# Performance work log

Measured on AMD Instinct MI355X. Metric: run time of the kernel, lower is better.

The kernel has to match this reference:

```python
import jax, jax.numpy as jnp
import numpy as np

N = 4096
D = 256
TAU = 0.8
LAM = 0.5
K0, K1 = 64, 128


def setup_inputs() -> dict:
    key = jax.random.key(0)
    ks = jax.random.split(key, 20)
    s = 1.0 / np.sqrt(D)
    pos = (jax.random.uniform(ks[3], (N, N)) < 0.01).astype(jnp.float32)
    pos = pos.at[jnp.arange(N), jnp.arange(N)].set(1.0)  # guarantee a positive per row
    return {
        'z_mp': jax.random.normal(ks[0], (N, D), jnp.float32),
        'z_sc': jax.random.normal(ks[1], (N, D), jnp.float32),
        'feat': jax.random.normal(ks[2], (N, D), jnp.float32),
        'pos': pos,
        'im2c0': jax.random.randint(ks[4], (N,), 0, K0, jnp.int32),
        'im2c1': jax.random.randint(ks[5], (N,), 0, K1, jnp.int32),
        'centroids0': jax.random.normal(ks[6], (K0, D), jnp.float32),
        'centroids1': jax.random.normal(ks[7], (K1, D), jnp.float32),
        'density0': jax.random.uniform(ks[8], (K0,), jnp.float32) + 0.5,
        'density1': jax.random.uniform(ks[9], (K1,), jnp.float32) + 0.5,
        'pW1': jax.random.normal(ks[10], (D, D), jnp.float32) * s * 1.414,
        'pb1': jnp.zeros((D,), jnp.float32),
        'pW2': jax.random.normal(ks[11], (D, D), jnp.float32) * s * 1.414,
        'pb2': jnp.zeros((D,), jnp.float32),
        'mW1': jax.random.normal(ks[12], (D, D), jnp.float32) * s,
        'mb1': jnp.zeros((D,), jnp.float32),
        'mW2': jax.random.normal(ks[13], (D, D), jnp.float32) * s,
        'mb2': jnp.zeros((D,), jnp.float32),
    }


def _mlp(x, W1, b1, W2, b2):
    # nn.Linear -> ELU -> nn.Linear (torch Linear: x @ W.T + b)
    return jax.nn.elu(x @ W1.T + b1) @ W2.T + b2


def _sim(z1, z2, tau):
    n1 = jnp.linalg.norm(z1, axis=-1, keepdims=True)
    n2 = jnp.linalg.norm(z2, axis=-1, keepdims=True)
    return jnp.exp((z1 @ z2.T) / (n1 @ n2.T) / tau)


def _nce(sim_matrix, pos):
    m = sim_matrix / (sim_matrix.sum(axis=1, keepdims=True) + 1e-8)
    return -jnp.log((m * pos).sum(axis=-1)).mean()


def _pocl(z_anchor, z, im2cs, centroids, densities):
    n = z_anchor.shape[0]
    # weight[a,b] = #levels where a,b share a cluster (original: coo @ coo.T summed)
    sames = [(c[:, None] == c[None, :]).astype(z.dtype) for c in im2cs]
    weight = sames[0] + sames[1]
    node_prototypes = jnp.zeros_like(z)
    loss = jnp.float32(0.0)
    for same, im2c, protos, dens in zip(sames, im2cs, centroids, densities):
        # original aliases weight_clus = weight, so masking accumulates in-place
        weight = weight * same
        c = (weight @ z) / weight.sum(axis=1)[:, None]
        node_prototypes = node_prototypes + 0.1 * c
        phi = dens[im2c]
        pos_p = jnp.exp((z_anchor * node_prototypes).sum(axis=1) / phi)
        neg_p = jnp.exp((z_anchor @ protos.T) / dens).mean(axis=1) * n
        loss = loss + (-jnp.log(pos_p / neg_p)).mean()
    return loss / len(im2cs)


def reference(z_mp, z_sc, feat, pos, im2c0, im2c1, centroids0, centroids1,
              density0, density1, pW1, pb1, pW2, pb2, mW1, mb1, mW2, mb2):
    z_proj_mp = _mlp(z_mp, pW1, pb1, pW2, pb2)
    z_proj_sc = _mlp(z_sc, pW1, pb1, pW2, pb2)
    m_mp2sc = _sim(z_proj_mp, z_proj_sc, TAU)
    lori_mp = _nce(m_mp2sc, pos)
    lori_sc = _nce(m_mp2sc.T, pos)
    proto_loss = _pocl(z_sc, z_mp, [im2c0, im2c1],
                       [centroids0, centroids1], [density0, density1])
    mp_intra = _mlp(z_mp, mW1, mb1, mW2, mb2)
    loss_intramp = _nce(_sim(mp_intra, mp_intra, 0.05), pos)
    proj_mp_feat = _mlp(z_mp, pW1, pb1, pW2, pb2)
    proj_feat = _mlp(feat, pW1, pb1, pW2, pb2)
    lori_mpfeat = _nce(_sim(proj_mp_feat, proj_feat, TAU), pos)
    lori_featmp = _nce(_sim(proj_feat, proj_mp_feat, TAU), pos)
    return (LAM * lori_mp + (1 - LAM) * lori_sc + 0.3 * loss_intramp
            + proto_loss + 0.01 * lori_mpfeat + 0.01 * lori_featmp)
```

## Files before the change

### kernel.cpp

```cpp
#include <hip/hip_runtime.h>
#include <math.h>


#define NROWS 4096
#define DIM   256
#define ND    ((size_t)NROWS * DIM)

typedef unsigned short u16;
typedef unsigned int   u32;
typedef unsigned long long u64;
typedef __attribute__((ext_vector_type(8))) short bf16x8;
typedef __attribute__((ext_vector_type(4))) float f32x4;

__device__ __forceinline__ u16 f2bf(float f) {
    u32 u = __float_as_uint(f);
    return (u16)((u + 0x7fffu + ((u >> 16) & 1u)) >> 16);
}
__device__ __forceinline__ float bf2f(u16 h) {
    return __uint_as_float(((u32)h) << 16);
}

__device__ __forceinline__ void gload16(const u16* g, u16* l) {
    __builtin_amdgcn_global_load_lds(
        (const __attribute__((address_space(1))) u32*)g,
        (__attribute__((address_space(3))) u32*)l, 16, 0, 0);
}

template<int ROWS>
__device__ __forceinline__ void stage_panel(const u16* P, int kk, u16* S, int tid) {
#pragma unroll
    for (int p = 0; p < ROWS / 64; ++p) {
        const int ch = p * 256 + tid, row = ch >> 2, seg = ch & 3;
        gload16(P + (size_t)row * DIM + kk + seg * 8, &S[ch * 8]);
    }
}

__device__ __forceinline__ void wait_lgkm0() {
    asm volatile("s_waitcnt lgkmcnt(0)" ::: "memory");
    __builtin_amdgcn_sched_barrier(0);
}
template<int N> __device__ __forceinline__ void wait_vm() {
    if constexpr (N == 0)      asm volatile("s_waitcnt vmcnt(0)" ::: "memory");
    else if constexpr (N == 3) asm volatile("s_waitcnt vmcnt(3)" ::: "memory");
    else if constexpr (N == 4) asm volatile("s_waitcnt vmcnt(4)" ::: "memory");
}

struct PreArgs {
    const float* in0; const float* in1; const float* in2;
    const float* w0; const float* w1; const float* w2; const float* w3;
    const float* c0; const float* c1;
    const float* pos; const float* z_mp;
    const int* im0; const int* im1;
};
__global__ __launch_bounds__(256) void fused_pre(PreArgs p,
                                                 u16* __restrict__ INb,
                                                 u16* __restrict__ Wb,
                                                 u16* __restrict__ CB,
                                                 u64* __restrict__ bits,
                                                 float* __restrict__ S01,
                                                 float* __restrict__ cnt01)
{
    const int b = blockIdx.x, tid = threadIdx.x;
    if (b < 3072) {
        const int z = b >> 10;
        const float* s = z == 0 ? p.in0 : (z == 1 ? p.in1 : p.in2);
        const int i = (b & 1023) * 256 + tid;
        const float4 v = ((const float4*)s)[i];
        ushort4 o;
        o.x = f2bf(v.x); o.y = f2bf(v.y); o.z = f2bf(v.z); o.w = f2bf(v.w);
        ((ushort4*)(INb + (size_t)z * ND))[i] = o;
    } else if (b < 3328) {
        const int q = b - 3072, wi = q >> 6;
        const float* s = wi == 0 ? p.w0 : (wi == 1 ? p.w1 : (wi == 2 ? p.w2 : p.w3));
        const int i = (q & 63) * 256 + tid;
        const float4 v = ((const float4*)s)[i];
        ushort4 o;
        o.x = f2bf(v.x); o.y = f2bf(v.y); o.z = f2bf(v.z); o.w = f2bf(v.w);
        ((ushort4*)(Wb + (size_t)wi * 65536))[i] = o;
    } else if (b < 3376) {
        const int i = (b - 3328) * 256 + tid;
        const float4 v = (i < 4096) ? ((const float4*)p.c0)[i]
                                    : ((const float4*)p.c1)[i - 4096];
        ushort4 o;
        o.x = f2bf(v.x); o.y = f2bf(v.y); o.z = f2bf(v.z); o.w = f2bf(v.w);
        ((ushort4*)CB)[i] = o;
    } else if (b < 7472) {
        const int i = b - 3376;
        const int w = tid >> 6, l = tid & 63;
#pragma unroll
        for (int c = 0; c < 16; ++c) {
            const int j = c * 256 + w * 64 + l;
            const float v = p.pos[(size_t)i * NROWS + j];
            const u64 m = __ballot(v != 0.f);
            if (l == 0) bits[(size_t)i * 64 + c * 4 + w] = m;
        }
    } else {
        const int r = b - 7472;
        const int pp = p.im0[r] * 128 + p.im1[r];
        atomicAdd(&S01[(size_t)pp * DIM + tid], p.z_mp[(size_t)r * DIM + tid]);
        if (tid == 0) atomicAdd(&cnt01[pp], 1.f);
    }
}

template<int ACT, int REMAP, int SQ>
__global__ __launch_bounds__(256, 4) void mlp_mfma(const u16* __restrict__ IN,
                                                   const u16* __restrict__ Wp,
                                                   const u16* __restrict__ Wm,
                                                   const float* __restrict__ bp,
                                                   const float* __restrict__ bm,
                                                   u16* __restrict__ OUT,
                                                   float* __restrict__ SS)
{
    __shared__ __align__(16) u16 As[3][64 * 32];
    __shared__ __align__(16) u16 Bs[3][128 * 32];
    const int tid = threadIdx.x;
    const int bx = blockIdx.x, by = blockIdx.y;
    const bool intra = by >= 192;
    const int arow = (REMAP && intra) ? (by - 192) * 64 : by * 64;
    const u16* A = IN + (size_t)arow * DIM;
    const u16* B = (intra ? Wm : Wp) + (size_t)(bx * 128) * DIM;
    const float* bias = intra ? bm : bp;
    const int l = tid & 63, w = tid >> 6, wr = w >> 1, wc = w & 1;
    const int lr = l & 15, lk = l >> 4;

    f32x4 acc[2][4] = {};
    stage_panel<64>(A, 0, As[0], tid);
    stage_panel<128>(B, 0, Bs[0], tid);
    stage_panel<64>(A, 32, As[1], tid);
    stage_panel<128>(B, 32, Bs[1], tid);
    wait_vm<3>();
    __builtin_amdgcn_s_barrier();
#pragma unroll
    for (int t = 0; t < 8; ++t) {
        bf16x8 a[2], b[4];
#pragma unroll
        for (int mi = 0; mi < 2; ++mi)
            a[mi] = *(const bf16x8*)&As[t % 3][(wr * 32 + mi * 16 + lr) * 32 + lk * 8];
#pragma unroll
        for (int ni = 0; ni < 4; ++ni)
            b[ni] = *(const bf16x8*)&Bs[t % 3][(wc * 64 + ni * 16 + lr) * 32 + lk * 8];
        if (t < 6) {
            stage_panel<64>(A, (t + 2) * 32, As[(t + 2) % 3], tid);
            stage_panel<128>(B, (t + 2) * 32, Bs[(t + 2) % 3], tid);
        }
        wait_lgkm0();
#pragma unroll
        for (int mi = 0; mi < 2; ++mi)
#pragma unroll
            for (int ni = 0; ni < 4; ++ni)
                acc[mi][ni] = __builtin_amdgcn_mfma_f32_16x16x32_bf16(a[mi], b[ni], acc[mi][ni], 0, 0, 0);
        if (t < 6)      { wait_vm<3>(); __builtin_amdgcn_s_barrier(); }
        else if (t < 7) { wait_vm<0>(); __builtin_amdgcn_s_barrier(); }
    }

    const int j0 = bx * 128;
    float bv[4];
#pragma unroll
    for (int ni = 0; ni < 4; ++ni) bv[ni] = bias[j0 + wc * 64 + ni * 16 + lr];
#pragma unroll
    for (int mi = 0; mi < 2; ++mi)
#pragma unroll
        for (int r = 0; r < 4; ++r) {
            const int row = by * 64 + wr * 32 + mi * 16 + lk * 4 + r;
            float v4[4], sq = 0.f;
#pragma unroll
            for (int ni = 0; ni < 4; ++ni) {
                float v = acc[mi][ni][r] + bv[ni];
                if (ACT) v = v > 0.f ? v : expm1f(v);
                v4[ni] = v;
                sq += v * v;
            }
            if (SQ) {
#pragma unroll
                for (int m = 1; m < 16; m <<= 1) sq += __shfl_xor(sq, m);
                if (lr == 0) atomicAdd(&SS[row], sq);
            }
#pragma unroll
            for (int ni = 0; ni < 4; ++ni)
                OUT[(size_t)row * DIM + j0 + wc * 64 + ni * 16 + lr] = f2bf(v4[ni]);
        }
}

__global__ __launch_bounds__(256, 3) void simstat3c(const u16* __restrict__ PROJ,
                                                    const u64* __restrict__ bits,
                                                    const float* __restrict__ SS,
                                                    float* __restrict__ ST)
{
    const int bid = blockIdx.x;
    int z, by, bx;
    if (bid < 1024) {
        z = 0;
        const int x = bid & 7, j = bid >> 3;
        by = (x >> 1) * 8 + (j >> 4);
        bx = (x & 1) * 16 + (j & 15);
    } else if (bid < 1552) {
        z = 1;
        const int u = bid - 1024;
        const int t = (u & 7) * 66 + (u >> 3);
        int r = (int)((65.0f - sqrtf(4225.0f - 8.0f * (float)t)) * 0.5f);
        int off = 32 * r - (r * (r - 1)) / 2;
        if (t < off)                   { --r; off -= 33 - r; }
        else if (t >= off + (32 - r))  { off += 32 - r; ++r; }
        by = r; bx = r + (t - off);
    } else {
        z = 2;
        const int v = bid - 1552;
        const int x = v & 7, j = v >> 3;
        by = (x >> 1) * 8 + (j >> 4);
        bx = (x & 1) * 16 + (j & 15);
    }

    __shared__ __align__(16) u16 As[3][128 * 32];
    __shared__ __align__(16) u16 Bs[3][128 * 32];
    const int tid = threadIdx.x;
    int ao, bo;
    float* rsr; float* rsc;
    switch (z) {
        case 0:  ao = 0; bo = 1; rsr = ST + 0;     rsc = ST + 8192;  break;
        case 1:  ao = 3; bo = 3; rsr = ST + 16384; rsc = ST + 16384; break;
        default: ao = 0; bo = 2; rsr = ST + 24576; rsc = ST + 32768; break;
    }
    const float invtau = (z == 1) ? 20.f : 1.25f;
    const bool docol = (z != 1) || (bx > by);
    const int i0 = by * 128, j0 = bx * 128;
    const u16* A = PROJ + (size_t)ao * ND + (size_t)i0 * DIM;
    const u16* B = PROJ + (size_t)bo * ND + (size_t)j0 * DIM;
    const int l = tid & 63, w = tid >> 6, wr = w >> 1, wc = w & 1;
    const int lr = l & 15, lk = l >> 4;

    f32x4 acc[4][4] = {};
    stage_panel<128>(A, 0, As[0], tid);
    stage_panel<128>(B, 0, Bs[0], tid);
    stage_panel<128>(A, 32, As[1], tid);
    stage_panel<128>(B, 32, Bs[1], tid);
    wait_vm<4>();
    __builtin_amdgcn_s_barrier();
#pragma unroll
    for (int t = 0; t < 8; ++t) {
        bf16x8 a[4], b[4];
#pragma unroll
        for (int mi = 0; mi < 4; ++mi)
            a[mi] = *(const bf16x8*)&As[t % 3][(wr * 64 + mi * 16 + lr) * 32 + lk * 8];
#pragma unroll
        for (int ni = 0; ni < 4; ++ni)
            b[ni] = *(const bf16x8*)&Bs[t % 3][(wc * 64 + ni * 16 + lr) * 32 + lk * 8];
        if (t < 6) {
            stage_panel<128>(A, (t + 2) * 32, As[(t + 2) % 3], tid);
            stage_panel<128>(B, (t + 2) * 32, Bs[(t + 2) % 3], tid);
        }
        wait_lgkm0();
#pragma unroll
        for (int mi = 0; mi < 4; ++mi)
#pragma unroll
            for (int ni = 0; ni < 4; ++ni)
                acc[mi][ni] = __builtin_amdgcn_mfma_f32_16x16x32_bf16(a[mi], b[ni], acc[mi][ni], 0, 0, 0);
        if (t < 6)      { wait_vm<4>(); __builtin_amdgcn_s_barrier(); }
        else if (t < 7) { wait_vm<0>(); __builtin_amdgcn_s_barrier(); }
    }

    const float* ssa = SS + ao * 4096;
    const float* ssb = SS + bo * 4096;
    float ri[4][4], rj[4];
#pragma unroll
    for (int mi = 0; mi < 4; ++mi)
#pragma unroll
        for (int r = 0; r < 4; ++r)
            ri[mi][r] = rsqrtf(ssa[i0 + wr * 64 + mi * 16 + lk * 4 + r]) * invtau;
#pragma unroll
    for (int ni = 0; ni < 4; ++ni)
        rj[ni] = rsqrtf(ssb[j0 + wc * 64 + ni * 16 + lr]);
#pragma unroll
    for (int mi = 0; mi < 4; ++mi)
#pragma unroll
        for (int ni = 0; ni < 4; ++ni)
#pragma unroll
            for (int r = 0; r < 4; ++r)
                acc[mi][ni][r] = __expf(acc[mi][ni][r] * ri[mi][r] * rj[ni]);

#pragma unroll
    for (int mi = 0; mi < 4; ++mi)
#pragma unroll
        for (int r = 0; r < 4; ++r) {
            const int i = i0 + wr * 64 + mi * 16 + lk * 4 + r;
            const u64 pw = bits[(size_t)i * 64 + bx * 2 + wc];
            float rsum = 0.f, psum = 0.f;
#pragma unroll
            for (int ni = 0; ni < 4; ++ni) {
                const float ev = acc[mi][ni][r];
                rsum += ev;
                psum += ((pw >> (ni * 16 + lr)) & 1ull) ? ev : 0.f;
            }
#pragma unroll
            for (int m = 1; m < 16; m <<= 1) {
                rsum += __shfl_xor(rsum, m);
                psum += __shfl_xor(psum, m);
            }
            if (lr == 0) {
                atomicAdd(&rsr[i], rsum);
                atomicAdd(&rsr[4096 + i], psum);
            }
        }

    if (docol) {
#pragma unroll
        for (int ni = 0; ni < 4; ++ni) {
            const int j = j0 + wc * 64 + ni * 16 + lr;
            const u64 pw = bits[(size_t)j * 64 + by * 2 + wr];
            float csum = 0.f, qsum = 0.f;
#pragma unroll
            for (int mi = 0; mi < 4; ++mi)
#pragma unroll
                for (int r = 0; r < 4; ++r) {
                    const float ev = acc[mi][ni][r];
                    csum += ev;
                    qsum += ((pw >> (mi * 16 + lk * 4 + r)) & 1ull) ? ev : 0.f;
                }
            csum += __shfl_xor(csum, 16); csum += __shfl_xor(csum, 32);
            qsum += __shfl_xor(qsum, 16); qsum += __shfl_xor(qsum, 32);
            if (lk == 0) {
                atomicAdd(&rsc[j], csum);
                atomicAdd(&rsc[4096 + j], qsum);
            }
        }
    }
}

__global__ __launch_bounds__(256, 4) void gcent_mfma(const u16* __restrict__ Zb,
                                                     const u16* __restrict__ CB,
                                                     float* __restrict__ G)
{
    __shared__ __align__(16) u16 As[3][128 * 32];
    __shared__ __align__(16) u16 Bs[3][64 * 32];
    const int tid = threadIdx.x;
    const int bx = blockIdx.x, by = blockIdx.y;
    const int i0 = by * 128, j0 = bx * 64;
    const u16* A = Zb + (size_t)i0 * DIM;
    const u16* B = CB + (size_t)j0 * DIM;
    const int l = tid & 63, w = tid >> 6, wr = w >> 1, wc = w & 1;
    const int lr = l & 15, lk = l >> 4;

    f32x4 acc[4][2] = {};
    stage_panel<128>(A, 0, As[0], tid);
    stage_panel<64>(B, 0, Bs[0], tid);
    stage_panel<128>(A, 32, As[1], tid);
    stage_panel<64>(B, 32, Bs[1], tid);
    wait_vm<3>();
    __builtin_amdgcn_s_barrier();
#pragma unroll
    for (int t = 0; t < 8; ++t) {
        bf16x8 a[4], b[2];
#pragma unroll
        for (int mi = 0; mi < 4; ++mi)
            a[mi] = *(const bf16x8*)&As[t % 3][(wr * 64 + mi * 16 + lr) * 32 + lk * 8];
#pragma unroll
        for (int ni = 0; ni < 2; ++ni)
            b[ni] = *(const bf16x8*)&Bs[t % 3][(wc * 32 + ni * 16 + lr) * 32 + lk * 8];
        if (t < 6) {
            stage_panel<128>(A, (t + 2) * 32, As[(t + 2) % 3], tid);
            stage_panel<64>(B, (t + 2) * 32, Bs[(t + 2) % 3], tid);
        }
        wait_lgkm0();
#pragma unroll
        for (int mi = 0; mi < 4; ++mi)
#pragma unroll
            for (int ni = 0; ni < 2; ++ni)
                acc[mi][ni] = __builtin_amdgcn_mfma_f32_16x16x32_bf16(a[mi], b[ni], acc[mi][ni], 0, 0, 0);
        if (t < 6)      { wait_vm<3>(); __builtin_amdgcn_s_barrier(); }
        else if (t < 7) { wait_vm<0>(); __builtin_amdgcn_s_barrier(); }
    }

#pragma unroll
    for (int mi = 0; mi < 4; ++mi)
#pragma unroll
        for (int r = 0; r < 4; ++r) {
            const int row = i0 + wr * 64 + mi * 16 + lk * 4 + r;
#pragma unroll
            for (int ni = 0; ni < 2; ++ni)
                G[(size_t)row * 192 + j0 + wc * 32 + ni * 16 + lr] = acc[mi][ni][r];
        }
}

__global__ __launch_bounds__(256) void reduce_pairs(const float* __restrict__ S01,
                                                    const float* __restrict__ cnt01,
                                                    float* __restrict__ S0,
                                                    float* __restrict__ cnt0)
{
    const int k0 = blockIdx.x, d = threadIdx.x;
    float s = 0.f;
    for (int k1 = 0; k1 < 128; ++k1)
        s += S01[(size_t)(k0 * 128 + k1) * DIM + d];
    S0[(size_t)k0 * DIM + d] = s;
    __shared__ float c[128];
    if (d < 128) c[d] = cnt01[k0 * 128 + d];
    __syncthreads();
    if (d == 0) {
        float t = 0.f;
        for (int i = 0; i < 128; ++i) t += c[i];
        cnt0[k0] = t;
    }
}

__global__ __launch_bounds__(256) void pocl_row(const float* __restrict__ z_sc,
                                                const int* __restrict__ i0a,
                                                const int* __restrict__ i1a,
                                                const float* __restrict__ S0,
                                                const float* __restrict__ S01,
                                                const float* __restrict__ cnt0,
                                                const float* __restrict__ cnt01,
                                                const float* __restrict__ G,
                                                const float* __restrict__ d0,
                                                const float* __restrict__ d1,
                                                float* __restrict__ L1,
                                                float* __restrict__ L2)
{
    const int w = threadIdx.x >> 6, l = threadIdx.x & 63;
    const int a = blockIdx.x * 4 + w;
    const int k0 = i0a[a], k1 = i1a[a];
    const int p = k0 * 128 + k1;
    const float n0 = cnt0[k0], n01 = cnt01[p];
    const float inv1 = 1.f / (n0 + n01), inv2 = 1.f / n01;
    const float4 s0  = *(const float4*)&S0[(size_t)k0 * DIM + l * 4];
    const float4 s01 = *(const float4*)&S01[(size_t)p * DIM + l * 4];
    const float4 zd  = *(const float4*)&z_sc[(size_t)a * DIM + l * 4];

    float dot1 = 0.f, dot2 = 0.f;
    {
        const float c1x = (s0.x + s01.x) * inv1, c2x = s01.x * inv2;
        const float c1y = (s0.y + s01.y) * inv1, c2y = s01.y * inv2;
        const float c1z = (s0.z + s01.z) * inv1, c2z = s01.z * inv2;
        const float c1w = (s0.w + s01.w) * inv1, c2w = s01.w * inv2;
        dot1 = zd.x * c1x + zd.y * c1y + zd.z * c1z + zd.w * c1w;
        dot2 = zd.x * (c1x + c2x) + zd.y * (c1y + c2y) + zd.z * (c1z + c2z) + zd.w * (c1w + c2w);
    }
    dot1 *= 0.1f; dot2 *= 0.1f;
#pragma unroll
    for (int m = 1; m < 64; m <<= 1) {
        dot1 += __shfl_xor(dot1, m);
        dot2 += __shfl_xor(dot2, m);
    }

    const float x0 = G[(size_t)a * 192 + l] / d0[l];
    float M0 = x0;
#pragma unroll
    for (int m = 1; m < 64; m <<= 1) M0 = fmaxf(M0, __shfl_xor(M0, m));
    float e0 = __expf(x0 - M0);
#pragma unroll
    for (int m = 1; m < 64; m <<= 1) e0 += __shfl_xor(e0, m);

    const float x1a = G[(size_t)a * 192 + 64 + l] / d1[l];
    const float x1b = G[(size_t)a * 192 + 128 + l] / d1[64 + l];
    float M1 = fmaxf(x1a, x1b);
#pragma unroll
    for (int m = 1; m < 64; m <<= 1) M1 = fmaxf(M1, __shfl_xor(M1, m));
    float e1 = __expf(x1a - M1) + __expf(x1b - M1);
#pragma unroll
    for (int m = 1; m < 64; m <<= 1) e1 += __shfl_xor(e1, m);

    if (l == 0) {
        const float lneg1 = M0 + logf(e0) - logf(64.f)  + logf(4096.f);
        const float lneg2 = M1 + logf(e1) - logf(128.f) + logf(4096.f);
        L1[a] = lneg1 - dot1 / d0[k0];
        L2[a] = lneg2 - dot2 / d1[k1];
    }
}

__global__ __launch_bounds__(256) void final_reduce(const float* __restrict__ st,
                                                    const float* __restrict__ L1,
                                                    const float* __restrict__ L2,
                                                    float* __restrict__ out)
{
    const int t = threadIdx.x;
    const float* rs0 = st + 0;      const float* pr0 = st + 4096;
    const float* rs1 = st + 8192;   const float* pr1 = st + 12288;
    const float* rs2 = st + 16384;  const float* pr2 = st + 20480;
    const float* rs3 = st + 24576;  const float* pr3 = st + 28672;
    const float* rs4 = st + 32768;  const float* pr4 = st + 36864;

    float acc = 0.f;
    for (int i = t; i < NROWS; i += 256) {
        const float lmp = logf(rs0[i] + 1e-8f) - logf(pr0[i]);
        const float lsc = logf(rs1[i] + 1e-8f) - logf(pr1[i]);
        const float lin = logf(rs2[i] + 1e-8f) - logf(pr2[i]);
        const float lmf = logf(rs3[i] + 1e-8f) - logf(pr3[i]);
        const float lfm = logf(rs4[i] + 1e-8f) - logf(pr4[i]);
        acc += 0.5f * (lmp + lsc) + 0.3f * lin
             + 0.01f * (lmf + lfm) + 0.5f * (L1[i] + L2[i]);
    }
    __shared__ float red[256];
    red[t] = acc; __syncthreads();
    for (int s = 128; s > 0; s >>= 1) {
        if (t < s) red[t] += red[t + s];
        __syncthreads();
    }
    if (t == 0) out[0] = red[0] * (1.f / 4096.f);
}

extern "C" void kernel_launch(void* const* d_in, const int* in_sizes, int n_in,
                              void* d_out, int out_size, void* d_ws, size_t ws_size,
                              hipStream_t stream)
{
    const float* z_mp = (const float*)d_in[0];
    const float* z_sc = (const float*)d_in[1];
    const float* feat = (const float*)d_in[2];
    const float* pos  = (const float*)d_in[3];
    const int*   im0  = (const int*)d_in[4];
    const int*   im1  = (const int*)d_in[5];
    const float* c0   = (const float*)d_in[6];
    const float* c1   = (const float*)d_in[7];
    const float* d0   = (const float*)d_in[8];
    const float* d1   = (const float*)d_in[9];
    const float* pW1  = (const float*)d_in[10];
    const float* pb1  = (const float*)d_in[11];
    const float* pW2  = (const float*)d_in[12];
    const float* pb2  = (const float*)d_in[13];
    const float* mW1  = (const float*)d_in[14];
    const float* mb1  = (const float*)d_in[15];
    const float* mW2  = (const float*)d_in[16];
    const float* mb2  = (const float*)d_in[17];
    float* out = (float*)d_out;
    float* ws  = (float*)d_ws;
    (void)in_sizes; (void)n_in; (void)out_size; (void)ws_size;

    float* ST   = ws;
    float* S0f  = ST + 40960;
    float* CN0  = S0f + 16384;
    float* CN01 = CN0 + 64;
    float* S01f = CN01 + 8192;
    float* SS   = S01f + (size_t)8192 * DIM;
    float* ZEND = SS + 16384;
    float* G    = ZEND;
    float* L1   = G + (size_t)NROWS * 192;
    float* L2   = L1 + NROWS;
    u64*  bits  = (u64*)(L2 + NROWS);
    u16*  INb   = (u16*)(bits + (size_t)NROWS * 64);
    u16*  Hb    = INb + 3 * ND;
    u16*  PROJ  = Hb + 4 * ND;
    u16*  Wb    = PROJ + 4 * ND;
    u16*  CB    = Wb + 4 * 65536;

    hipMemsetAsync(ws, 0, (size_t)(ZEND - ws) * sizeof(float), stream);

    const dim3 blk(256);

    PreArgs pa{z_mp, z_sc, feat, pW1, pW2, mW1, mW2, c0, c1, pos, z_mp, im0, im1};
    fused_pre<<<11568, blk, 0, stream>>>(pa, INb, Wb, CB, bits, S01f, CN01);

    mlp_mfma<1, 1, 0><<<dim3(2, 256), blk, 0, stream>>>(INb, Wb, Wb + 2 * 65536,
                                                        pb1, mb1, Hb, nullptr);
    mlp_mfma<0, 0, 1><<<dim3(2, 256), blk, 0, stream>>>(Hb, Wb + 65536, Wb + 3 * 65536,
                                                        pb2, mb2, PROJ, SS);

    simstat3c<<<2576, blk, 0, stream>>>(PROJ, bits, SS, ST);

    reduce_pairs<<<64, blk, 0, stream>>>(S01f, CN01, S0f, CN0);
    gcent_mfma<<<dim3(3, 32), blk, 0, stream>>>(INb + ND, CB, G);
    pocl_row<<<1024, blk, 0, stream>>>(z_sc, im0, im1, S0f, S01f, CN0, CN01,
                                       G, d0, d1, L1, L2);

    final_reduce<<<1, blk, 0, stream>>>(ST, L1, L2, out);
}
```

Measured before the change: 156.7 us.

## Merge independent small kernels into two combined launches and use DPP row sums

```diff
diff --git a/kernel.cpp b/kernel.cpp
--- a/kernel.cpp
+++ b/kernel.cpp
@@ -43,6 +43,14 @@
     if constexpr (N == 0)      asm volatile("s_waitcnt vmcnt(0)" ::: "memory");
     else if constexpr (N == 3) asm volatile("s_waitcnt vmcnt(3)" ::: "memory");
     else if constexpr (N == 4) asm volatile("s_waitcnt vmcnt(4)" ::: "memory");
+}
+
+__device__ __forceinline__ float rowsum16(float v) {
+    v += __int_as_float(__builtin_amdgcn_update_dpp(0, __float_as_int(v), 0x118, 0xf, 0xf, true));
+    v += __int_as_float(__builtin_amdgcn_update_dpp(0, __float_as_int(v), 0x114, 0xf, 0xf, true));
+    v += __int_as_float(__builtin_amdgcn_update_dpp(0, __float_as_int(v), 0x112, 0xf, 0xf, true));
+    v += __int_as_float(__builtin_amdgcn_update_dpp(0, __float_as_int(v), 0x111, 0xf, 0xf, true));
+    return v;
 }
 
 struct PreArgs {
@@ -103,18 +111,17 @@
 }
 
 template<int ACT, int REMAP, int SQ>
-__global__ __launch_bounds__(256, 4) void mlp_mfma(const u16* __restrict__ IN,
-                                                   const u16* __restrict__ Wp,
-                                                   const u16* __restrict__ Wm,
-                                                   const float* __restrict__ bp,
-                                                   const float* __restrict__ bm,
-                                                   u16* __restrict__ OUT,
-                                                   float* __restrict__ SS)
-{
-    __shared__ __align__(16) u16 As[3][64 * 32];
-    __shared__ __align__(16) u16 Bs[3][128 * 32];
-    const int tid = threadIdx.x;
-    const int bx = blockIdx.x, by = blockIdx.y;
+__device__ __forceinline__ void mlp_body(int bx, int by, u16* lds, int tid,
+                                         const u16* __restrict__ IN,
+                                         const u16* __restrict__ Wp,
+                                         const u16* __restrict__ Wm,
+                                         const float* __restrict__ bp,
+                                         const float* __restrict__ bm,
+                                         u16* __restrict__ OUT,
+                                         float* __restrict__ SS)
+{
+    u16* As = lds;
+    u16* Bs = lds + 3 * 2048;
     const bool intra = by >= 192;
     const int arow = (REMAP && intra) ? (by - 192) * 64 : by * 64;
     const u16* A = IN + (size_t)arow * DIM;
@@ -124,10 +131,10 @@
     const int lr = l & 15, lk = l >> 4;
 
     f32x4 acc[2][4] = {};
-    stage_panel<64>(A, 0, As[0], tid);
-    stage_panel<128>(B, 0, Bs[0], tid);
-    stage_panel<64>(A, 32, As[1], tid);
-    stage_panel<128>(B, 32, Bs[1], tid);
+    stage_panel<64>(A, 0, As, tid);
+    stage_panel<128>(B, 0, Bs, tid);
+    stage_panel<64>(A, 32, As + 2048, tid);
+    stage_panel<128>(B, 32, Bs + 4096, tid);
     wait_vm<3>();
     __builtin_amdgcn_s_barrier();
 #pragma unroll
@@ -135,13 +142,13 @@
         bf16x8 a[2], b[4];
 #pragma unroll
         for (int mi = 0; mi < 2; ++mi)
-            a[mi] = *(const bf16x8*)&As[t % 3][(wr * 32 + mi * 16 + lr) * 32 + lk * 8];
+            a[mi] = *(const bf16x8*)&As[(t % 3) * 2048 + (wr * 32 + mi * 16 + lr) * 32 + lk * 8];
 #pragma unroll
         for (int ni = 0; ni < 4; ++ni)
-            b[ni] = *(const bf16x8*)&Bs[t % 3][(wc * 64 + ni * 16 + lr) * 32 + lk * 8];
+            b[ni] = *(const bf16x8*)&Bs[(t % 3) * 4096 + (wc * 64 + ni * 16 + lr) * 32 + lk * 8];
         if (t < 6) {
-            stage_panel<64>(A, (t + 2) * 32, As[(t + 2) % 3], tid);
-            stage_panel<128>(B, (t + 2) * 32, Bs[(t + 2) % 3], tid);
+            stage_panel<64>(A, (t + 2) * 32, As + ((t + 2) % 3) * 2048, tid);
+            stage_panel<128>(B, (t + 2) * 32, Bs + ((t + 2) % 3) * 4096, tid);
         }
         wait_lgkm0();
 #pragma unroll
@@ -171,14 +178,187 @@
                 sq += v * v;
             }
             if (SQ) {
-#pragma unroll
-                for (int m = 1; m < 16; m <<= 1) sq += __shfl_xor(sq, m);
-                if (lr == 0) atomicAdd(&SS[row], sq);
+                sq = rowsum16(sq);
+                if (lr == 15) atomicAdd(&SS[row], sq);
             }
 #pragma unroll
             for (int ni = 0; ni < 4; ++ni)
                 OUT[(size_t)row * DIM + j0 + wc * 64 + ni * 16 + lr] = f2bf(v4[ni]);
         }
+}
+
+__device__ __forceinline__ void gcent_body(int bx, int by, u16* lds, int tid,
+                                           const u16* __restrict__ Zb,
+                                           const u16* __restrict__ CB,
+                                           float* __restrict__ G)
+{
+    u16* As = lds;
+    u16* Bs = lds + 3 * 4096;
+    const int i0 = by * 128, j0 = bx * 64;
+    const u16* A = Zb + (size_t)i0 * DIM;
+    const u16* B = CB + (size_t)j0 * DIM;
+    const int l = tid & 63, w = tid >> 6, wr = w >> 1, wc = w & 1;
+    const int lr = l & 15, lk = l >> 4;
+
+    f32x4 acc[4][2] = {};
+    stage_panel<128>(A, 0, As, tid);
+    stage_panel<64>(B, 0, Bs, tid);
+    stage_panel<128>(A, 32, As + 4096, tid);
+    stage_panel<64>(B, 32, Bs + 2048, tid);
+    wait_vm<3>();
+    __builtin_amdgcn_s_barrier();
+#pragma unroll
+    for (int t = 0; t < 8; ++t) {
+        bf16x8 a[4], b[2];
+#pragma unroll
+        for (int mi = 0; mi < 4; ++mi)
+            a[mi] = *(const bf16x8*)&As[(t % 3) * 4096 + (wr * 64 + mi * 16 + lr) * 32 + lk * 8];
+#pragma unroll
+        for (int ni = 0; ni < 2; ++ni)
+            b[ni] = *(const bf16x8*)&Bs[(t % 3) * 2048 + (wc * 32 + ni * 16 + lr) * 32 + lk * 8];
+        if (t < 6) {
+            stage_panel<128>(A, (t + 2) * 32, As + ((t + 2) % 3) * 4096, tid);
+            stage_panel<64>(B, (t + 2) * 32, Bs + ((t + 2) % 3) * 2048, tid);
+        }
+        wait_lgkm0();
+#pragma unroll
+        for (int mi = 0; mi < 4; ++mi)
+#pragma unroll
+            for (int ni = 0; ni < 2; ++ni)
+                acc[mi][ni] = __builtin_amdgcn_mfma_f32_16x16x32_bf16(a[mi], b[ni], acc[mi][ni], 0, 0, 0);
+        if (t < 6)      { wait_vm<3>(); __builtin_amdgcn_s_barrier(); }
+        else if (t < 7) { wait_vm<0>(); __builtin_amdgcn_s_barrier(); }
+    }
+
+#pragma unroll
+    for (int mi = 0; mi < 4; ++mi)
+#pragma unroll
+        for (int r = 0; r < 4; ++r) {
+            const int row = i0 + wr * 64 + mi * 16 + lk * 4 + r;
+#pragma unroll
+            for (int ni = 0; ni < 2; ++ni)
+                G[(size_t)row * 192 + j0 + wc * 32 + ni * 16 + lr] = acc[mi][ni][r];
+        }
+}
+
+__device__ __forceinline__ void pocl_body(int blk, int tid,
+                                          const float* __restrict__ z_sc,
+                                          const int* __restrict__ i0a,
+                                          const int* __restrict__ i1a,
+                                          const float* __restrict__ S0,
+                                          const float* __restrict__ S01,
+                                          const float* __restrict__ cnt0,
+                                          const float* __restrict__ cnt01,
+                                          const float* __restrict__ G,
+                                          const float* __restrict__ d0,
+                                          const float* __restrict__ d1,
+                                          float* __restrict__ L1,
+                                          float* __restrict__ L2)
+{
+    const int w = tid >> 6, l = tid & 63;
+    const int a = blk * 4 + w;
+    const int k0 = i0a[a], k1 = i1a[a];
+    const int p = k0 * 128 + k1;
+    const float n0 = cnt0[k0], n01 = cnt01[p];
+    const float inv1 = 1.f / (n0 + n01), inv2 = 1.f / n01;
+    const float4 s0  = *(const float4*)&S0[(size_t)k0 * DIM + l * 4];
+    const float4 s01 = *(const float4*)&S01[(size_t)p * DIM + l * 4];
+    const float4 zd  = *(const float4*)&z_sc[(size_t)a * DIM + l * 4];
+
+    float dot1 = 0.f, dot2 = 0.f;
+    {
+        const float c1x = (s0.x + s01.x) * inv1, c2x = s01.x * inv2;
+        const float c1y = (s0.y + s01.y) * inv1, c2y = s01.y * inv2;
+        const float c1z = (s0.z + s01.z) * inv1, c2z = s01.z * inv2;
+        const float c1w = (s0.w + s01.w) * inv1, c2w = s01.w * inv2;
+        dot1 = zd.x * c1x + zd.y * c1y + zd.z * c1z + zd.w * c1w;
+        dot2 = zd.x * (c1x + c2x) + zd.y * (c1y + c2y) + zd.z * (c1z + c2z) + zd.w * (c1w + c2w);
+    }
+    dot1 *= 0.1f; dot2 *= 0.1f;
+#pragma unroll
+    for (int m = 1; m < 64; m <<= 1) {
+        dot1 += __shfl_xor(dot1, m);
+        dot2 += __shfl_xor(dot2, m);
+    }
+
+    const float x0 = G[(size_t)a * 192 + l] / d0[l];
+    float M0 = x0;
+#pragma unroll
+    for (int m = 1; m < 64; m <<= 1) M0 = fmaxf(M0, __shfl_xor(M0, m));
+    float e0 = __expf(x0 - M0);
+#pragma unroll
+    for (int m = 1; m < 64; m <<= 1) e0 += __shfl_xor(e0, m);
+
+    const float x1a = G[(size_t)a * 192 + 64 + l] / d1[l];
+    const float x1b = G[(size_t)a * 192 + 128 + l] / d1[64 + l];
+    float M1 = fmaxf(x1a, x1b);
+#pragma unroll
+    for (int m = 1; m < 64; m <<= 1) M1 = fmaxf(M1, __shfl_xor(M1, m));
+    float e1 = __expf(x1a - M1) + __expf(x1b - M1);
+#pragma unroll
+    for (int m = 1; m < 64; m <<= 1) e1 += __shfl_xor(e1, m);
+
+    if (l == 0) {
+        const float lneg1 = M0 + logf(e0) - logf(64.f)  + logf(4096.f);
+        const float lneg2 = M1 + logf(e1) - logf(128.f) + logf(4096.f);
+        L1[a] = lneg1 - dot1 / d0[k0];
+        L2[a] = lneg2 - dot2 / d1[k1];
+    }
+}
+
+struct C1Args {
+    const u16* INb; const u16* Wb; const u16* CB;
+    const float* pb1; const float* mb1;
+    u16* Hb; float* G;
+    const float* S01; const float* cnt01; float* S0; float* cnt0;
+};
+__global__ __launch_bounds__(256, 4) void combo1(C1Args a)
+{
+    extern __shared__ u16 smem[];
+    const int b = blockIdx.x, tid = threadIdx.x;
+    if (b < 512) {
+        mlp_body<1, 1, 0>(b & 1, b >> 1, smem, tid, a.INb, a.Wb, a.Wb + 2 * 65536,
+                          a.pb1, a.mb1, a.Hb, nullptr);
+    } else if (b < 608) {
+        const int q = b - 512;
+        gcent_body(q % 3, q / 3, smem, tid, a.INb + ND, a.CB, a.G);
+    } else {
+        const int k0 = b - 608, d = tid;
+        float s = 0.f;
+        for (int k1 = 0; k1 < 128; ++k1)
+            s += a.S01[(size_t)(k0 * 128 + k1) * DIM + d];
+        a.S0[(size_t)k0 * DIM + d] = s;
+        float* c = (float*)smem;
+        if (d < 128) c[d] = a.cnt01[k0 * 128 + d];
+        __syncthreads();
+        if (d == 0) {
+            float t = 0.f;
+            for (int i = 0; i < 128; ++i) t += c[i];
+            a.cnt0[k0] = t;
+        }
+    }
+}
+
+struct C2Args {
+    const u16* Hb; const u16* Wb;
+    const float* pb2; const float* mb2;
+    u16* PROJ; float* SS;
+    const float* z_sc; const int* im0; const int* im1;
+    const float* S0; const float* S01; const float* cnt0; const float* cnt01;
+    const float* G; const float* d0; const float* d1;
+    float* L1; float* L2;
+};
+__global__ __launch_bounds__(256, 4) void combo2(C2Args a)
+{
+    extern __shared__ u16 smem[];
+    const int b = blockIdx.x, tid = threadIdx.x;
+    if (b < 512) {
+        mlp_body<0, 0, 1>(b & 1, b >> 1, smem, tid, a.Hb, a.Wb + 65536,
+                          a.Wb + 3 * 65536, a.pb2, a.mb2, a.PROJ, a.SS);
+    } else {
+        pocl_body(b - 512, tid, a.z_sc, a.im0, a.im1, a.S0, a.S01, a.cnt0,
+                  a.cnt01, a.G, a.d0, a.d1, a.L1, a.L2);
+    }
 }
 
 __global__ __launch_bounds__(256, 3) void simstat3c(const u16* __restrict__ PROJ,
@@ -290,12 +470,9 @@
                 rsum += ev;
                 psum += ((pw >> (ni * 16 + lr)) & 1ull) ? ev : 0.f;
             }
-#pragma unroll
-            for (int m = 1; m < 16; m <<= 1) {
-                rsum += __shfl_xor(rsum, m);
-                psum += __shfl_xor(psum, m);
-            }
-            if (lr == 0) {
+            rsum = rowsum16(rsum);
+            psum = rowsum16(psum);
+            if (lr == 15) {
                 atomicAdd(&rsr[i], rsum);
                 atomicAdd(&rsr[4096 + i], psum);
             }
@@ -322,145 +499,6 @@
                 atomicAdd(&rsc[4096 + j], qsum);
             }
         }
-    }
-}
-
-__global__ __launch_bounds__(256, 4) void gcent_mfma(const u16* __restrict__ Zb,
-                                                     const u16* __restrict__ CB,
-                                                     float* __restrict__ G)
-{
-    __shared__ __align__(16) u16 As[3][128 * 32];
-    __shared__ __align__(16) u16 Bs[3][64 * 32];
-    const int tid = threadIdx.x;
-    const int bx = blockIdx.x, by = blockIdx.y;
-    const int i0 = by * 128, j0 = bx * 64;
-    const u16* A = Zb + (size_t)i0 * DIM;
-    const u16* B = CB + (size_t)j0 * DIM;
-    const int l = tid & 63, w = tid >> 6, wr = w >> 1, wc = w & 1;
-    const int lr = l & 15, lk = l >> 4;
-
-    f32x4 acc[4][2] = {};
-    stage_panel<128>(A, 0, As[0], tid);
-    stage_panel<64>(B, 0, Bs[0], tid);
-    stage_panel<128>(A, 32, As[1], tid);
-    stage_panel<64>(B, 32, Bs[1], tid);
-    wait_vm<3>();
-    __builtin_amdgcn_s_barrier();
-#pragma unroll
-    for (int t = 0; t < 8; ++t) {
-        bf16x8 a[4], b[2];
-#pragma unroll
-        for (int mi = 0; mi < 4; ++mi)
-            a[mi] = *(const bf16x8*)&As[t % 3][(wr * 64 + mi * 16 + lr) * 32 + lk * 8];
-#pragma unroll
-        for (int ni = 0; ni < 2; ++ni)
-            b[ni] = *(const bf16x8*)&Bs[t % 3][(wc * 32 + ni * 16 + lr) * 32 + lk * 8];
-        if (t < 6) {
-            stage_panel<128>(A, (t + 2) * 32, As[(t + 2) % 3], tid);
-            stage_panel<64>(B, (t + 2) * 32, Bs[(t + 2) % 3], tid);
-        }
-        wait_lgkm0();
-#pragma unroll
-        for (int mi = 0; mi < 4; ++mi)
-#pragma unroll
-            for (int ni = 0; ni < 2; ++ni)
-                acc[mi][ni] = __builtin_amdgcn_mfma_f32_16x16x32_bf16(a[mi], b[ni], acc[mi][ni], 0, 0, 0);
-        if (t < 6)      { wait_vm<3>(); __builtin_amdgcn_s_barrier(); }
-        else if (t < 7) { wait_vm<0>(); __builtin_amdgcn_s_barrier(); }
-    }
-
-#pragma unroll
-    for (int mi = 0; mi < 4; ++mi)
-#pragma unroll
-        for (int r = 0; r < 4; ++r) {
-            const int row = i0 + wr * 64 + mi * 16 + lk * 4 + r;
-#pragma unroll
-            for (int ni = 0; ni < 2; ++ni)
-                G[(size_t)row * 192 + j0 + wc * 32 + ni * 16 + lr] = acc[mi][ni][r];
-        }
-}
-
-__global__ __launch_bounds__(256) void reduce_pairs(const float* __restrict__ S01,
-                                                    const float* __restrict__ cnt01,
-                                                    float* __restrict__ S0,
-                                                    float* __restrict__ cnt0)
-{
-    const int k0 = blockIdx.x, d = threadIdx.x;
-    float s = 0.f;
-    for (int k1 = 0; k1 < 128; ++k1)
-        s += S01[(size_t)(k0 * 128 + k1) * DIM + d];
-    S0[(size_t)k0 * DIM + d] = s;
-    __shared__ float c[128];
-    if (d < 128) c[d] = cnt01[k0 * 128 + d];
-    __syncthreads();
-    if (d == 0) {
-        float t = 0.f;
-        for (int i = 0; i < 128; ++i) t += c[i];
-        cnt0[k0] = t;
-    }
-}
-
-__global__ __launch_bounds__(256) void pocl_row(const float* __restrict__ z_sc,
-                                                const int* __restrict__ i0a,
-                                                const int* __restrict__ i1a,
-                                                const float* __restrict__ S0,
-                                                const float* __restrict__ S01,
-                                                const float* __restrict__ cnt0,
-                                                const float* __restrict__ cnt01,
-                                                const float* __restrict__ G,
-                                                const float* __restrict__ d0,
-                                                const float* __restrict__ d1,
-                                                float* __restrict__ L1,
-                                                float* __restrict__ L2)
-{
-    const int w = threadIdx.x >> 6, l = threadIdx.x & 63;
-    const int a = blockIdx.x * 4 + w;
-    const int k0 = i0a[a], k1 = i1a[a];
-    const int p = k0 * 128 + k1;
-    const float n0 = cnt0[k0], n01 = cnt01[p];
-    const float inv1 = 1.f / (n0 + n01), inv2 = 1.f / n01;
-    const float4 s0  = *(const float4*)&S0[(size_t)k0 * DIM + l * 4];
-    const float4 s01 = *(const float4*)&S01[(size_t)p * DIM + l * 4];
-    const float4 zd  = *(const float4*)&z_sc[(size_t)a * DIM + l * 4];
-
-    float dot1 = 0.f, dot2 = 0.f;
-    {
-        const float c1x = (s0.x + s01.x) * inv1, c2x = s01.x * inv2;
-        const float c1y = (s0.y + s01.y) * inv1, c2y = s01.y * inv2;
-        const float c1z = (s0.z + s01.z) * inv1, c2z = s01.z * inv2;
-        const float c1w = (s0.w + s01.w) * inv1, c2w = s01.w * inv2;
-        dot1 = zd.x * c1x + zd.y * c1y + zd.z * c1z + zd.w * c1w;
-        dot2 = zd.x * (c1x + c2x) + zd.y * (c1y + c2y) + zd.z * (c1z + c2z) + zd.w * (c1w + c2w);
-    }
-    dot1 *= 0.1f; dot2 *= 0.1f;
-#pragma unroll
-    for (int m = 1; m < 64; m <<= 1) {
-        dot1 += __shfl_xor(dot1, m);
-        dot2 += __shfl_xor(dot2, m);
-    }
-
-    const float x0 = G[(size_t)a * 192 + l] / d0[l];
-    float M0 = x0;
-#pragma unroll
-    for (int m = 1; m < 64; m <<= 1) M0 = fmaxf(M0, __shfl_xor(M0, m));
-    float e0 = __expf(x0 - M0);
-#pragma unroll
-    for (int m = 1; m < 64; m <<= 1) e0 += __shfl_xor(e0, m);
-
-    const float x1a = G[(size_t)a * 192 + 64 + l] / d1[l];
-    const float x1b = G[(size_t)a * 192 + 128 + l] / d1[64 + l];
-    float M1 = fmaxf(x1a, x1b);
-#pragma unroll
-    for (int m = 1; m < 64; m <<= 1) M1 = fmaxf(M1, __shfl_xor(M1, m));
-    float e1 = __expf(x1a - M1) + __expf(x1b - M1);
-#pragma unroll
-    for (int m = 1; m < 64; m <<= 1) e1 += __shfl_xor(e1, m);
-
-    if (l == 0) {
-        const float lneg1 = M0 + logf(e0) - logf(64.f)  + logf(4096.f);
-        const float lneg2 = M1 + logf(e1) - logf(128.f) + logf(4096.f);
-        L1[a] = lneg1 - dot1 / d0[k0];
-        L2[a] = lneg2 - dot2 / d1[k1];
     }
 }
 
@@ -541,21 +579,19 @@
     hipMemsetAsync(ws, 0, (size_t)(ZEND - ws) * sizeof(float), stream);
 
     const dim3 blk(256);
+    const size_t lds_bytes = 36 * 1024;
 
     PreArgs pa{z_mp, z_sc, feat, pW1, pW2, mW1, mW2, c0, c1, pos, z_mp, im0, im1};
     fused_pre<<<11568, blk, 0, stream>>>(pa, INb, Wb, CB, bits, S01f, CN01);
 
-    mlp_mfma<1, 1, 0><<<dim3(2, 256), blk, 0, stream>>>(INb, Wb, Wb + 2 * 65536,
-                                                        pb1, mb1, Hb, nullptr);
-    mlp_mfma<0, 0, 1><<<dim3(2, 256), blk, 0, stream>>>(Hb, Wb + 65536, Wb + 3 * 65536,
-                                                        pb2, mb2, PROJ, SS);
+    C1Args a1{INb, Wb, CB, pb1, mb1, Hb, G, S01f, CN01, S0f, CN0};
+    combo1<<<672, blk, lds_bytes, stream>>>(a1);
+
+    C2Args a2{Hb, Wb, pb2, mb2, PROJ, SS, z_sc, im0, im1,
+              S0f, S01f, CN0, CN01, G, d0, d1, L1, L2};
+    combo2<<<1536, blk, lds_bytes, stream>>>(a2);
 
     simstat3c<<<2576, blk, 0, stream>>>(PROJ, bits, SS, ST);
 
-    reduce_pairs<<<64, blk, 0, stream>>>(S01f, CN01, S0f, CN0);
-    gcent_mfma<<<dim3(3, 32), blk, 0, stream>>>(INb + ND, CB, G);
-    pocl_row<<<1024, blk, 0, stream>>>(z_sc, im0, im1, S0f, S01f, CN0, CN01,
-                                       G, d0, d1, L1, L2);
-
     final_reduce<<<1, blk, 0, stream>>>(ST, L1, L2, out);
 }
```

After: 140.9 us, median of 3. 10.1% less time.
